# Performance work log

Hardware: AMD Instinct MI355X
Metric: run time of the kernel (lower is better)

Reference implementation:

```python
import jax, jax.numpy as jnp
import numpy as np

IN_DIM = 18 * 2 * 1 * 536  # 19296
H = 512
OUT = 11
STEPS = 1024


def setup_inputs() -> dict:
    key = jax.random.key(0)
    ks = jax.random.split(key, 14)
    s = 0.02  # small init scale for stable LSTM dynamics
    f32 = jnp.float32
    return {
        "inputs": jax.random.normal(ks[0], (STEPS, IN_DIM), dtype=f32),
        "W_in": jax.random.normal(ks[1], (H, IN_DIM), dtype=f32) * s,
        "b_in": jnp.zeros((H,), dtype=f32),
        "Wih0": jax.random.normal(ks[2], (4 * H, H), dtype=f32) * s,
        "Whh0": jax.random.normal(ks[3], (4 * H, H), dtype=f32) * s,
        "bih0": jnp.zeros((4 * H,), dtype=f32),
        "bhh0": jnp.zeros((4 * H,), dtype=f32),
        "Wih1": jax.random.normal(ks[4], (4 * H, H), dtype=f32) * s,
        "Whh1": jax.random.normal(ks[5], (4 * H, H), dtype=f32) * s,
        "bih1": jnp.zeros((4 * H,), dtype=f32),
        "bhh1": jnp.zeros((4 * H,), dtype=f32),
        "W_out": jax.random.normal(ks[6], (OUT, H), dtype=f32) * s,
        "b_out": jnp.zeros((OUT,), dtype=f32),
    }


def _lstm_cell(gates, c):
    # PyTorch gate order: input, forget, cell(g), output
    i, f, g, o = jnp.split(gates, 4, axis=-1)
    c_new = jax.nn.sigmoid(f) * c + jax.nn.sigmoid(i) * jnp.tanh(g)
    h_new = jax.nn.sigmoid(o) * jnp.tanh(c_new)
    return h_new, c_new


def reference(inputs, W_in, b_in, Wih0, Whh0, bih0, bhh0,
              Wih1, Whh1, bih1, bhh1, W_out, b_out):
    # Input projection is time-independent -> batch it across all steps.
    x_proj = inputs @ W_in.T + b_in            # (STEPS, H)
    gx0 = x_proj @ Wih0.T + bih0               # (STEPS, 4H) precomputed layer-0 input gates

    def step(carry, gx0_t):
        h0, c0, h1, c1 = carry
        h0, c0 = _lstm_cell(gx0_t + h0 @ Whh0.T + bhh0, c0)
        h1, c1 = _lstm_cell(h0 @ Wih1.T + bih1 + h1 @ Whh1.T + bhh1, c1)
        return (h0, c0, h1, c1), h1

    z = jnp.zeros((H,), dtype=inputs.dtype)
    (h0, c0, h1, c1), hs = jax.lax.scan(step, (z, z, z, z), gx0)
    outputs = (hs @ W_out.T + b_out)[:, None, :]   # (STEPS, 1, OUT) == torch (steps, batch=1, 11)
    hn = jnp.stack([h0, h1])[:, None, :]           # (num_layers=2, batch=1, H)
    cn = jnp.stack([c0, c1])[:, None, :]
    return outputs, hn, cn
```

## Files before the change

kernel.cpp:

```cpp
#include <hip/hip_runtime.h>
#include <math.h>

typedef unsigned long long ull;
typedef unsigned int u32;
typedef unsigned short u16;
typedef _Float16 half2v __attribute__((ext_vector_type(2)));
typedef __bf16 bf16x8 __attribute__((ext_vector_type(8)));
typedef float f32x4 __attribute__((ext_vector_type(4)));

#define H 512
#define STEPS 1024
#define OUTN 11

__device__ __forceinline__ float sigm(float x) { return 1.f / (1.f + __expf(-x)); }
__device__ __forceinline__ ull ld_pair(const ull* p) {
  return __hip_atomic_load((ull*)p, __ATOMIC_RELAXED, __HIP_MEMORY_SCOPE_AGENT);
}
__device__ __forceinline__ void st_pair(ull* p, ull v) {
  __hip_atomic_store(p, v, __ATOMIC_RELAXED, __HIP_MEMORY_SCOPE_AGENT);
}
__device__ __forceinline__ float dot2acc(half2v a, half2v b, float c) {
#if __has_builtin(__builtin_amdgcn_fdot2)
  return __builtin_amdgcn_fdot2(a, b, c, false);
#else
  return c + (float)a.x * (float)b.x + (float)a.y * (float)b.y;
#endif
}
__device__ __forceinline__ u16 f16bits(float x) {
  return __builtin_bit_cast(u16, (_Float16)x);
}
__device__ __forceinline__ half2v bch2(u32 u) { return __builtin_bit_cast(half2v, u); }

__device__ __forceinline__ u32 split_bf16(float x) {
  u32 u = __float_as_uint(x);
  u32 rh = (u + 0x7FFFu + ((u >> 16) & 1u)) & 0xFFFF0000u;
  float hf = __uint_as_float(rh);
  float lo = x - hf;
  u32 ul = __float_as_uint(lo);
  u32 rl = (ul + 0x7FFFu + ((ul >> 16) & 1u)) & 0xFFFF0000u;
  return (rh >> 16) | rl;
}

__global__ void cvt_split(float* __restrict__ A, float* __restrict__ B, int nA, int n4) {
  int idx = blockIdx.x * 256 + threadIdx.x;
  if (idx >= n4) return;
  int base = idx * 4;
  float* p = (base < nA) ? (A + base) : (B + (base - nA));
  float4 v = *(float4*)p;
  u32 r0 = split_bf16(v.x), r1 = split_bf16(v.y), r2 = split_bf16(v.z), r3 = split_bf16(v.w);
  uint4 o = make_uint4(r0, r1, r2, r3);
  *(uint4*)p = o;
}

__global__ __launch_bounds__(256, 2)
void gemm_hilo(const u32* __restrict__ A2, const u32* __restrict__ B2,
               float* __restrict__ C, int M, int N, int K)
{
  __shared__ __align__(16) u16 Ah[64 * 32], Al[64 * 32], Bh[64 * 32], Bl[64 * 32];
  const int z = blockIdx.z;
  const int zstart = z * 151;
  const int nsteps = (z < 3) ? 151 : 150;
  const int mt = blockIdx.x * 64, nt = blockIdx.y * 64;
  const int tid = threadIdx.x;
  const int row = tid >> 2, cg = (tid & 3) * 8;
  const int wave = tid >> 6, lane = tid & 63;
  const int wm = (wave & 1) * 32, wn = (wave >> 1) * 32;
  const int quad = lane >> 4, l16 = lane & 15;

  f32x4 acc[2][2];
#pragma unroll
  for (int i = 0; i < 2; ++i)
#pragma unroll
    for (int j = 0; j < 2; ++j) acc[i][j] = (f32x4)0.f;

  for (int s = 0; s < nsteps; ++s) {
    const int kb = (zstart + s) * 32;
    {
      const u32* ap = A2 + (size_t)(mt + row) * K + kb + cg;
      const u32* bp = B2 + (size_t)(nt + row) * K + kb + cg;
      uint4 a0 = *(const uint4*)ap, a1 = *(const uint4*)(ap + 4);
      uint4 b0 = *(const uint4*)bp, b1 = *(const uint4*)(bp + 4);
      uint4 hi, lo;
      hi = make_uint4((a0.x & 0xFFFF) | (a0.y << 16), (a0.z & 0xFFFF) | (a0.w << 16),
                      (a1.x & 0xFFFF) | (a1.y << 16), (a1.z & 0xFFFF) | (a1.w << 16));
      lo = make_uint4((a0.x >> 16) | (a0.y & 0xFFFF0000u), (a0.z >> 16) | (a0.w & 0xFFFF0000u),
                      (a1.x >> 16) | (a1.y & 0xFFFF0000u), (a1.z >> 16) | (a1.w & 0xFFFF0000u));
      *(uint4*)&Ah[row * 32 + cg] = hi;
      *(uint4*)&Al[row * 32 + cg] = lo;
      hi = make_uint4((b0.x & 0xFFFF) | (b0.y << 16), (b0.z & 0xFFFF) | (b0.w << 16),
                      (b1.x & 0xFFFF) | (b1.y << 16), (b1.z & 0xFFFF) | (b1.w << 16));
      lo = make_uint4((b0.x >> 16) | (b0.y & 0xFFFF0000u), (b0.z >> 16) | (b0.w & 0xFFFF0000u),
                      (b1.x >> 16) | (b1.y & 0xFFFF0000u), (b1.z >> 16) | (b1.w & 0xFFFF0000u));
      *(uint4*)&Bh[row * 32 + cg] = hi;
      *(uint4*)&Bl[row * 32 + cg] = lo;
    }
    __syncthreads();
    bf16x8 ah[2], al[2], bh[2], bl[2];
#pragma unroll
    for (int mf = 0; mf < 2; ++mf) {
      int r = (wm + mf * 16 + l16) * 32 + quad * 8;
      ah[mf] = *reinterpret_cast<const bf16x8*>(&Ah[r]);
      al[mf] = *reinterpret_cast<const bf16x8*>(&Al[r]);
    }
#pragma unroll
    for (int nf = 0; nf < 2; ++nf) {
      int r = (wn + nf * 16 + l16) * 32 + quad * 8;
      bh[nf] = *reinterpret_cast<const bf16x8*>(&Bh[r]);
      bl[nf] = *reinterpret_cast<const bf16x8*>(&Bl[r]);
    }
#pragma unroll
    for (int mf = 0; mf < 2; ++mf)
#pragma unroll
      for (int nf = 0; nf < 2; ++nf) {
        acc[mf][nf] = __builtin_amdgcn_mfma_f32_16x16x32_bf16(ah[mf], bh[nf], acc[mf][nf], 0, 0, 0);
        acc[mf][nf] = __builtin_amdgcn_mfma_f32_16x16x32_bf16(ah[mf], bl[nf], acc[mf][nf], 0, 0, 0);
        acc[mf][nf] = __builtin_amdgcn_mfma_f32_16x16x32_bf16(al[mf], bh[nf], acc[mf][nf], 0, 0, 0);
      }
    __syncthreads();
  }

#pragma unroll
  for (int mf = 0; mf < 2; ++mf)
#pragma unroll
    for (int nf = 0; nf < 2; ++nf)
#pragma unroll
      for (int r = 0; r < 4; ++r) {
        int rw = mt + wm + mf * 16 + quad * 4 + r;
        int cl = nt + wn + nf * 16 + l16;
        atomicAdd(&C[(size_t)rw * N + cl], acc[mf][nf][r]);
      }
}

#define GBM 64
#define GBN 64
#define GBK 64
#define GLD 76

__global__ __launch_bounds__(256, 2)
void gemm_nt(const float* __restrict__ A, const float* __restrict__ B,
             float* __restrict__ C, const float* __restrict__ bias,
             int M, int N, int K)
{
  __shared__ float As[GBM][GLD];
  __shared__ float Bs[GBN][GLD];
  const int mt = blockIdx.x, nt = blockIdx.y;
  const int tid = threadIdx.x;
  const int tx = tid & 15, ty = tid >> 4;

  float acc[4][4] = {{0.f}};

  for (int kb = 0; kb < K; kb += GBK) {
#pragma unroll
    for (int i = 0; i < 4; ++i) {
      int r = ty + i * 16;
      int gk = kb + tx * 4;
      *(float4*)&As[r][tx * 4] = *(const float4*)(A + (size_t)(mt * GBM + r) * K + gk);
      *(float4*)&Bs[r][tx * 4] = *(const float4*)(B + (size_t)(nt * GBN + r) * K + gk);
    }
    __syncthreads();
#pragma unroll
    for (int k4 = 0; k4 < GBK; k4 += 4) {
      float4 a[4], b[4];
#pragma unroll
      for (int i = 0; i < 4; ++i) a[i] = *(const float4*)&As[ty * 4 + i][k4];
#pragma unroll
      for (int j = 0; j < 4; ++j) b[j] = *(const float4*)&Bs[tx * 4 + j][k4];
#pragma unroll
      for (int i = 0; i < 4; ++i)
#pragma unroll
        for (int j = 0; j < 4; ++j) {
          acc[i][j] = fmaf(a[i].x, b[j].x, acc[i][j]);
          acc[i][j] = fmaf(a[i].y, b[j].y, acc[i][j]);
          acc[i][j] = fmaf(a[i].z, b[j].z, acc[i][j]);
          acc[i][j] = fmaf(a[i].w, b[j].w, acc[i][j]);
        }
    }
    __syncthreads();
  }

#pragma unroll
  for (int i = 0; i < 4; ++i) {
    int m = mt * GBM + ty * 4 + i;
#pragma unroll
    for (int j = 0; j < 4; ++j) {
      int n = nt * GBN + tx * 4 + j;
      C[(size_t)m * N + n] = acc[i][j] + bias[n];
    }
  }
}

__global__ void init_xproj(float* __restrict__ xp, const float* __restrict__ b_in) {
  int i = blockIdx.x * 256 + threadIdx.x;
  xp[i] = b_in[i & (H - 1)];
}

__global__ void out_proj(const float* __restrict__ hs1, const float* __restrict__ Wout,
                         const float* __restrict__ bout, float* __restrict__ out) {
  int idx = blockIdx.x * 256 + threadIdx.x;
  if (idx >= STEPS * OUTN) return;
  int t = idx / OUTN, o = idx - t * OUTN;
  const float* h = hs1 + t * H;
  const float* wr = Wout + o * H;
  float acc = 0.f;
#pragma unroll 4
  for (int i = 0; i < H; i += 4) {
    float4 hv = *(const float4*)(h + i);
    float4 wv = *(const float4*)(wr + i);
    acc = fmaf(hv.x, wv.x, acc);
    acc = fmaf(hv.y, wv.y, acc);
    acc = fmaf(hv.z, wv.z, acc);
    acc = fmaf(hv.w, wv.w, acc);
  }
  out[idx] = acc + bout[o];
}

#define NC0 24
#define NC1 16
#define RD 8

__global__ __launch_bounds__(512, 1)
void lstm_chains(const float* __restrict__ gx0,
                 const float* __restrict__ Whh0, const float* __restrict__ bhh0,
                 const float* __restrict__ Wih1, const float* __restrict__ Whh1,
                 const float* __restrict__ bih1, const float* __restrict__ bhh1,
                 float* __restrict__ hs1, float* __restrict__ out,
                 ull* __restrict__ mb0, ull* __restrict__ mb1,
                 int* __restrict__ flags1)
{
  const int wg = blockIdx.x;
  const int tid = threadIdx.x;
  const bool role0 = (wg < 8);

  __shared__ __align__(16) u32 hl_u[512];
  __shared__ __align__(16) float gbuf[256];
  __shared__ __align__(16) float gxb[256];
  __shared__ __align__(16) u32 pbuf[32];

  half2v wgt[8][16];
  float bias[8];
  int rg, ch;

  if (role0) {
    rg = tid >> 4; ch = tid & 15;
    int g = rg >> 3, lub = (rg & 7) * 8;
    int growb = (g << 9) + (wg << 6) + lub;
    const float* wb = Whh0 + (size_t)growb * H + ch * 32;
#pragma unroll
    for (int r = 0; r < 8; ++r) {
      const float* wr = wb + (size_t)r * H;
#pragma unroll
      for (int j4 = 0; j4 < 8; ++j4) {
        float4 f = *(const float4*)(wr + j4 * 4);
        wgt[r][2 * j4]     = half2v{(_Float16)f.x, (_Float16)f.y};
        wgt[r][2 * j4 + 1] = half2v{(_Float16)f.z, (_Float16)f.w};
      }
      bias[r] = bhh0[growb + r];
    }
  } else {
    rg = tid >> 5; ch = tid & 31;
    int g = rg >> 2, lub = (rg & 3) * 8;
    int growb = (g << 9) + ((wg - 8) << 5) + lub;
    const float* wb = (ch < 16) ? (Whh1 + (size_t)growb * H + ch * 32)
                                : (Wih1 + (size_t)growb * H + (ch - 16) * 32);
#pragma unroll
    for (int r = 0; r < 8; ++r) {
      const float* wr = wb + (size_t)r * H;
#pragma unroll
      for (int j4 = 0; j4 < 8; ++j4) {
        float4 f = *(const float4*)(wr + j4 * 4);
        wgt[r][2 * j4]     = half2v{(_Float16)f.x, (_Float16)f.y};
        wgt[r][2 * j4 + 1] = half2v{(_Float16)f.z, (_Float16)f.w};
      }
      bias[r] = bih1[growb + r] + bhh1[growb + r];
    }
  }

  float c_state = 0.f, h_last = 0.f;

  if (role0) {
    const int w = wg;
    for (int t = 0; t < STEPS; ++t) {
      if (tid >= 256) {
        int j = tid - 256;
        gxb[j] = gx0[t * 2048 + ((j >> 6) << 9) + (w << 6) + (j & 63)];
        if (j < 16 && (t & 3) == 0 && t > 0) {
          int need = t - 4, f;
          const int* fp = flags1 + ((w << 4) + j) * 16;
          do {
            f = __hip_atomic_load(fp, __ATOMIC_RELAXED, __HIP_MEMORY_SCOPE_AGENT);
          } while (f < need);
        }
      } else {
        const ull* src = mb0 + ((((w << 3) | ((t + RD - 1) & (RD - 1)))) << 8) + tid;
        ull p;
        do { p = ld_pair(src); } while ((unsigned)(p >> 32) != (unsigned)t);
        hl_u[tid] = (u32)p;
      }
      __syncthreads();

      float accv[8];
#pragma unroll
      for (int r = 0; r < 8; ++r) accv[r] = 0.f;
      {
        const u32* hp = hl_u + (ch << 4);
        uint4 q0 = *(const uint4*)hp;
        uint4 q1 = *(const uint4*)(hp + 4);
        uint4 q2 = *(const uint4*)(hp + 8);
        uint4 q3 = *(const uint4*)(hp + 12);
        half2v h2[16] = {bch2(q0.x), bch2(q0.y), bch2(q0.z), bch2(q0.w),
                         bch2(q1.x), bch2(q1.y), bch2(q1.z), bch2(q1.w),
                         bch2(q2.x), bch2(q2.y), bch2(q2.z), bch2(q2.w),
                         bch2(q3.x), bch2(q3.y), bch2(q3.z), bch2(q3.w)};
#pragma unroll
        for (int j = 0; j < 16; ++j)
#pragma unroll
          for (int r = 0; r < 8; ++r)
            accv[r] = dot2acc(wgt[r][j], h2[j], accv[r]);
      }
#pragma unroll
      for (int o = 1; o < 16; o <<= 1)
#pragma unroll
        for (int r = 0; r < 8; ++r)
          accv[r] += __shfl_xor(accv[r], o);
      if (ch == 0) {
        float4 ga = *(const float4*)&gxb[rg * 8];
        float4 gb = *(const float4*)&gxb[rg * 8 + 4];
        float4 o0 = make_float4(accv[0] + bias[0] + ga.x, accv[1] + bias[1] + ga.y,
                                accv[2] + bias[2] + ga.z, accv[3] + bias[3] + ga.w);
        float4 o1 = make_float4(accv[4] + bias[4] + gb.x, accv[5] + bias[5] + gb.y,
                                accv[6] + bias[6] + gb.z, accv[7] + bias[7] + gb.w);
        *(float4*)&gbuf[rg * 8] = o0;
        *(float4*)&gbuf[rg * 8 + 4] = o1;
      }
      __syncthreads();

      if (tid < 64) {
        float gi = gbuf[tid], gf = gbuf[64 + tid], gg = gbuf[128 + tid], go = gbuf[192 + tid];
        c_state = sigm(gf) * c_state + sigm(gi) * tanhf(gg);
        float hv = sigm(go) * tanhf(c_state);
        float hnb = __shfl_down(hv, 1);
        if ((tid & 1) == 0)
          pbuf[tid >> 1] = (u32)f16bits(hv) | ((u32)f16bits(hnb) << 16);
        h_last = hv;
      }
      __syncthreads();

      if (tid >= 256) {
        const int q = (tid >> 6) - 4;
        const int l = tid & 63, half = l >> 5, p = l & 31;
        const ull pay = ((ull)(unsigned)(t + 1) << 32) | (ull)pbuf[p];
        const int slot = t & (RD - 1);
        const int base = (w << 5) + p;
        const int cb = q + (half << 2);
        st_pair(mb0 + (((cb << 3) | slot) << 8) + base, pay);
        st_pair(mb0 + ((((8 + cb) << 3) | slot) << 8) + base, pay);
        st_pair(mb0 + ((((16 + cb) << 3) | slot) << 8) + base, pay);
      }
    }
  } else {
    const int v = wg - 8;
    for (int tau = 1; tau <= STEPS; ++tau) {
      const int t = tau - 1;
      if (tid < 256) {
        const ull* q1 = mb1 + ((((v << 3) | ((t + RD - 1) & (RD - 1)))) << 8) + tid;
        ull p;
        do { p = ld_pair(q1); } while ((unsigned)(p >> 32) != (unsigned)t);
        hl_u[tid] = (u32)p;
      } else {
        const ull* q0 = mb0 + (((((8 + v) << 3) | (t & (RD - 1)))) << 8) + (tid - 256);
        ull p;
        do { p = ld_pair(q0); } while ((unsigned)(p >> 32) != (unsigned)(t + 1));
        hl_u[tid] = (u32)p;
      }
      __syncthreads();

      float accv[8];
#pragma unroll
      for (int r = 0; r < 8; ++r) accv[r] = 0.f;
      {
        const u32* hp = hl_u + (ch << 4);
        uint4 q0 = *(const uint4*)hp;
        uint4 q1 = *(const uint4*)(hp + 4);
        uint4 q2 = *(const uint4*)(hp + 8);
        uint4 q3 = *(const uint4*)(hp + 12);
        half2v h2[16] = {bch2(q0.x), bch2(q0.y), bch2(q0.z), bch2(q0.w),
                         bch2(q1.x), bch2(q1.y), bch2(q1.z), bch2(q1.w),
                         bch2(q2.x), bch2(q2.y), bch2(q2.z), bch2(q2.w),
                         bch2(q3.x), bch2(q3.y), bch2(q3.z), bch2(q3.w)};
#pragma unroll
        for (int j = 0; j < 16; ++j)
#pragma unroll
          for (int r = 0; r < 8; ++r)
            accv[r] = dot2acc(wgt[r][j], h2[j], accv[r]);
      }
#pragma unroll
      for (int o = 1; o < 32; o <<= 1)
#pragma unroll
        for (int r = 0; r < 8; ++r)
          accv[r] += __shfl_xor(accv[r], o);
      if (ch == 0) {
        float4 o0 = make_float4(accv[0] + bias[0], accv[1] + bias[1],
                                accv[2] + bias[2], accv[3] + bias[3]);
        float4 o1 = make_float4(accv[4] + bias[4], accv[5] + bias[5],
                                accv[6] + bias[6], accv[7] + bias[7]);
        *(float4*)&gbuf[rg * 8] = o0;
        *(float4*)&gbuf[rg * 8 + 4] = o1;
      }
      __syncthreads();

      if (tid < 32) {
        int u = (v << 5) + tid;
        float gi = gbuf[tid], gf = gbuf[32 + tid], gg = gbuf[64 + tid], go = gbuf[96 + tid];
        c_state = sigm(gf) * c_state + sigm(gi) * tanhf(gg);
        float hv = sigm(go) * tanhf(c_state);
        float hnb = __shfl_down(hv, 1);
        if ((tid & 1) == 0)
          pbuf[tid >> 1] = (u32)f16bits(hv) | ((u32)f16bits(hnb) << 16);
        h_last = hv;
        hs1[t * H + u] = hv;
      }
      if (((tau & 3) == 0) && tid >= 64 && tid < 72)
        __hip_atomic_store(flags1 + (((tid - 64) << 4) + v) * 16, tau,
                           __ATOMIC_RELAXED, __HIP_MEMORY_SCOPE_AGENT);
      __syncthreads();

      if (tid < 256) {
        const int q = tid >> 6;
        const int l = tid & 63, half = l >> 5, p = l & 31;
        if (p < 16) {
          const ull pay = ((ull)(unsigned)(t + 1) << 32) | (ull)pbuf[p];
          const int slot = t & (RD - 1);
          const int base = (v << 4) + p;
          const int cb = q + (half << 2);
          st_pair(mb1 + (((cb << 3) | slot) << 8) + base, pay);
          st_pair(mb1 + ((((8 + cb) << 3) | slot) << 8) + base, pay);
        }
      }
    }
  }

  if (role0) {
    if (tid < 64) {
      int u = (wg << 6) + tid;
      out[STEPS * OUTN + u] = h_last;
      out[STEPS * OUTN + 2 * H + u] = c_state;
    }
  } else {
    if (tid < 32) {
      int u = ((wg - 8) << 5) + tid;
      out[STEPS * OUTN + H + u] = h_last;
      out[STEPS * OUTN + 3 * H + u] = c_state;
    }
  }
}

extern "C" void kernel_launch(void* const* d_in, const int* in_sizes, int n_in,
                              void* d_out, int out_size, void* d_ws, size_t ws_size,
                              hipStream_t stream)
{
  (void)in_sizes; (void)n_in; (void)out_size; (void)ws_size;
  float* inputs = (float*)d_in[0];
  float* W_in   = (float*)d_in[1];
  const float* b_in   = (const float*)d_in[2];
  const float* Wih0   = (const float*)d_in[3];
  const float* Whh0   = (const float*)d_in[4];
  const float* bih0   = (const float*)d_in[5];
  const float* bhh0   = (const float*)d_in[6];
  const float* Wih1   = (const float*)d_in[7];
  const float* Whh1   = (const float*)d_in[8];
  const float* bih1   = (const float*)d_in[9];
  const float* bhh1   = (const float*)d_in[10];
  const float* W_out  = (const float*)d_in[11];
  const float* b_out  = (const float*)d_in[12];
  float* out = (float*)d_out;
  float* ws = (float*)d_ws;

  float* xp  = ws;
  float* gx0 = ws + 524288;
  float* hs1 = ws + 524288 + 2097152;
  char* syncb = (char*)(ws + 3145728);
  ull* mb0 = (ull*)syncb;
  ull* mb1 = (ull*)(syncb + 24 * 8 * 256 * 8);
  int* flags1 = (int*)(syncb + (24 + 16) * 8 * 256 * 8);

  hipMemsetAsync(syncb, 0, (24 + 16) * 8 * 256 * 8 + 8192, stream);

  {
    const int nA = STEPS * 19296;
    const int n4 = (nA + H * 19296) / 4;
    cvt_split<<<n4 / 256, 256, 0, stream>>>(inputs, W_in, nA, n4);
  }
  init_xproj<<<2048, 256, 0, stream>>>(xp, b_in);
  {
    dim3 g(16, 8, 4);
    gemm_hilo<<<g, 256, 0, stream>>>((const u32*)inputs, (const u32*)W_in, xp,
                                     1024, 512, 19296);
  }
  {
    dim3 g(16, 32, 1);
    gemm_nt<<<g, 256, 0, stream>>>(xp, Wih0, gx0, bih0, 1024, 2048, 512);
  }
  lstm_chains<<<24, 512, 0, stream>>>(gx0, Whh0, bhh0, Wih1, Whh1, bih1, bhh1,
                                      hs1, out, mb0, mb1, flags1);
  out_proj<<<44, 256, 0, stream>>>(hs1, W_out, b_out, out);
}
```

Baseline: 3.103 ms.

## Co-locate LSTM workgroups on one XCD and poll L2-local mailboxes

Launches 256 workgroups, reads each one's XCD id from a hardware register, and lets only the 24 workgroups on the most populated XCD take the LSTM roles while the rest exit. Producers also write every mailbox payload with plain stores that stay in the shared L2, and consumers poll that copy with sc0 loads, falling back to the agent-scope copy every few tries. The aim is to cut the cross-XCD coherence latency of each step handshake in the serial recurrence. It relies on undocumented register encoding and on at least 24 workgroups landing on one XCD and being co-resident; otherwise too few roles get filled and the kernel can deadlock.

```diff
diff --git a/kernel.cpp b/kernel.cpp
--- a/kernel.cpp
+++ b/kernel.cpp
@@ -19,6 +19,23 @@
 __device__ __forceinline__ void st_pair(ull* p, ull v) {
   __hip_atomic_store(p, v, __ATOMIC_RELAXED, __HIP_MEMORY_SCOPE_AGENT);
 }
+__device__ __forceinline__ void st_local(ull* p, ull v) {
+  asm volatile("global_store_dwordx2 %0, %1, off" :: "v"(p), "v"(v) : "memory");
+}
+__device__ __forceinline__ ull poll2(const ull* fast, const ull* slow, unsigned want) {
+  for (;;) {
+#pragma unroll 1
+    for (int s = 0; s < 6; ++s) {
+      ull r;
+      asm volatile("global_load_dwordx2 %0, %1, off sc0\n\ts_waitcnt vmcnt(0)"
+                   : "=v"(r) : "v"(fast) : "memory");
+      if ((unsigned)(r >> 32) == want) return r;
+    }
+    ull r = __hip_atomic_load((ull*)slow, __ATOMIC_RELAXED, __HIP_MEMORY_SCOPE_AGENT);
+    if ((unsigned)(r >> 32) == want) return r;
+  }
+}
+
 __device__ __forceinline__ float dot2acc(half2v a, half2v b, float c) {
 #if __has_builtin(__builtin_amdgcn_fdot2)
   return __builtin_amdgcn_fdot2(a, b, c, false);
@@ -217,6 +234,7 @@
 #define NC0 24
 #define NC1 16
 #define RD 8
+#define NWG 256
 
 __global__ __launch_bounds__(512, 1)
 void lstm_chains(const float* __restrict__ gx0,
@@ -225,10 +243,33 @@
                  const float* __restrict__ bih1, const float* __restrict__ bhh1,
                  float* __restrict__ hs1, float* __restrict__ out,
                  ull* __restrict__ mb0, ull* __restrict__ mb1,
-                 int* __restrict__ flags1)
+                 int* __restrict__ flags1, int* __restrict__ claim,
+                 ull* __restrict__ lmb0, ull* __restrict__ lmb1)
 {
-  const int wg = blockIdx.x;
   const int tid = threadIdx.x;
+  __shared__ int s_role;
+
+  if (tid == 0) {
+    u32 xid = ((u32)__builtin_amdgcn_s_getreg(63508)) & 7u;
+    __hip_atomic_fetch_add(&claim[xid * 16], 1, __ATOMIC_SEQ_CST, __HIP_MEMORY_SCOPE_AGENT);
+    __hip_atomic_fetch_add(&claim[128], 1, __ATOMIC_SEQ_CST, __HIP_MEMORY_SCOPE_AGENT);
+    while (__hip_atomic_load(&claim[128], __ATOMIC_SEQ_CST, __HIP_MEMORY_SCOPE_AGENT) < NWG)
+      __builtin_amdgcn_s_sleep(8);
+    int best = 0, bc = -1;
+    for (int i = 0; i < 8; ++i) {
+      int c = __hip_atomic_load(&claim[i * 16], __ATOMIC_SEQ_CST, __HIP_MEMORY_SCOPE_AGENT);
+      if (c > bc) { bc = c; best = i; }
+    }
+    int role = -1;
+    if ((int)xid == best) {
+      int s = __hip_atomic_fetch_add(&claim[144], 1, __ATOMIC_SEQ_CST, __HIP_MEMORY_SCOPE_AGENT);
+      if (s < 24) role = s;
+    }
+    s_role = role;
+  }
+  __syncthreads();
+  const int wg = s_role;
+  if (wg < 0) return;
   const bool role0 = (wg < 8);
 
   __shared__ __align__(16) u32 hl_u[512];
@@ -291,9 +332,8 @@
           } while (f < need);
         }
       } else {
-        const ull* src = mb0 + ((((w << 3) | ((t + RD - 1) & (RD - 1)))) << 8) + tid;
-        ull p;
-        do { p = ld_pair(src); } while ((unsigned)(p >> 32) != (unsigned)t);
+        const int idx = ((((w << 3) | ((t + RD - 1) & (RD - 1)))) << 8) + tid;
+        ull p = poll2(lmb0 + idx, mb0 + idx, (unsigned)t);
         hl_u[tid] = (u32)p;
       }
       __syncthreads();
@@ -352,9 +392,15 @@
         const int slot = t & (RD - 1);
         const int base = (w << 5) + p;
         const int cb = q + (half << 2);
-        st_pair(mb0 + (((cb << 3) | slot) << 8) + base, pay);
-        st_pair(mb0 + ((((8 + cb) << 3) | slot) << 8) + base, pay);
-        st_pair(mb0 + ((((16 + cb) << 3) | slot) << 8) + base, pay);
+        const int i0 = (((cb << 3) | slot) << 8) + base;
+        const int i1 = ((((8 + cb) << 3) | slot) << 8) + base;
+        const int i2 = ((((16 + cb) << 3) | slot) << 8) + base;
+        st_local(lmb0 + i0, pay);
+        st_local(lmb0 + i1, pay);
+        st_local(lmb0 + i2, pay);
+        st_pair(mb0 + i0, pay);
+        st_pair(mb0 + i1, pay);
+        st_pair(mb0 + i2, pay);
       }
     }
   } else {
@@ -362,14 +408,12 @@
     for (int tau = 1; tau <= STEPS; ++tau) {
       const int t = tau - 1;
       if (tid < 256) {
-        const ull* q1 = mb1 + ((((v << 3) | ((t + RD - 1) & (RD - 1)))) << 8) + tid;
-        ull p;
-        do { p = ld_pair(q1); } while ((unsigned)(p >> 32) != (unsigned)t);
+        const int idx = ((((v << 3) | ((t + RD - 1) & (RD - 1)))) << 8) + tid;
+        ull p = poll2(lmb1 + idx, mb1 + idx, (unsigned)t);
         hl_u[tid] = (u32)p;
       } else {
-        const ull* q0 = mb0 + (((((8 + v) << 3) | (t & (RD - 1)))) << 8) + (tid - 256);
-        ull p;
-        do { p = ld_pair(q0); } while ((unsigned)(p >> 32) != (unsigned)(t + 1));
+        const int idx = (((((8 + v) << 3) | (t & (RD - 1)))) << 8) + (tid - 256);
+        ull p = poll2(lmb0 + idx, mb0 + idx, (unsigned)(t + 1));
         hl_u[tid] = (u32)p;
       }
       __syncthreads();
@@ -432,8 +476,12 @@
           const int slot = t & (RD - 1);
           const int base = (v << 4) + p;
           const int cb = q + (half << 2);
-          st_pair(mb1 + (((cb << 3) | slot) << 8) + base, pay);
-          st_pair(mb1 + ((((8 + cb) << 3) | slot) << 8) + base, pay);
+          const int i0 = (((cb << 3) | slot) << 8) + base;
+          const int i1 = ((((8 + cb) << 3) | slot) << 8) + base;
+          st_local(lmb1 + i0, pay);
+          st_local(lmb1 + i1, pay);
+          st_pair(mb1 + i0, pay);
+          st_pair(mb1 + i1, pay);
         }
       }
     }
@@ -479,11 +527,14 @@
   float* gx0 = ws + 524288;
   float* hs1 = ws + 524288 + 2097152;
   char* syncb = (char*)(ws + 3145728);
-  ull* mb0 = (ull*)syncb;
-  ull* mb1 = (ull*)(syncb + 24 * 8 * 256 * 8);
-  int* flags1 = (int*)(syncb + (24 + 16) * 8 * 256 * 8);
-
-  hipMemsetAsync(syncb, 0, (24 + 16) * 8 * 256 * 8 + 8192, stream);
+  ull* mb0    = (ull*)syncb;
+  ull* mb1    = (ull*)(syncb + 393216);
+  int* flags1 = (int*)(syncb + 655360);
+  int* claim  = (int*)(syncb + 663552);
+  ull* lmb0   = (ull*)(syncb + 664576);
+  ull* lmb1   = (ull*)(syncb + 1057792);
+
+  hipMemsetAsync(syncb, 0, 1319936, stream);
 
   {
     const int nA = STEPS * 19296;
@@ -500,7 +551,7 @@
     dim3 g(16, 32, 1);
     gemm_nt<<<g, 256, 0, stream>>>(xp, Wih0, gx0, bih0, 1024, 2048, 512);
   }
-  lstm_chains<<<24, 512, 0, stream>>>(gx0, Whh0, bhh0, Wih1, Whh1, bih1, bhh1,
-                                      hs1, out, mb0, mb1, flags1);
+  lstm_chains<<<NWG, 512, 0, stream>>>(gx0, Whh0, bhh0, Wih1, Whh1, bih1, bhh1,
+                                       hs1, out, mb0, mb1, flags1, claim, lmb0, lmb1);
   out_proj<<<44, 256, 0, stream>>>(hs1, W_out, b_out, out);
 }
```

Result: slower. 3.530 ms (+13.8%).

## Fuse input GEMMs and LSTM chains into one persistent kernel with flag-gated overlap

Applied to the files above, without the earlier changes.

Merges the bf16 split conversion, bias init, input-projection GEMM, gate GEMM and the recurrent LSTM chains into a single persistent launch. 24 blocks run the recurrence while 232 worker blocks pull GEMM tiles from an atomic queue. The first time-slab of rows gets finer K-splitting so the recurrence can start early, and per-tile ready flags let the chains consume gx0 in 64-step chunks as it is produced. This aims to hide the long serial LSTM behind the projection work and remove launch gaps. The cost is spin-wait synchronisation, grid-wide barriers that rely on every block being co-resident, and more shared memory per block.

```diff
diff --git a/kernel.cpp b/kernel.cpp
--- a/kernel.cpp
+++ b/kernel.cpp
@@ -39,159 +39,6 @@
   u32 ul = __float_as_uint(lo);
   u32 rl = (ul + 0x7FFFu + ((ul >> 16) & 1u)) & 0xFFFF0000u;
   return (rh >> 16) | rl;
-}
-
-__global__ void cvt_split(float* __restrict__ A, float* __restrict__ B, int nA, int n4) {
-  int idx = blockIdx.x * 256 + threadIdx.x;
-  if (idx >= n4) return;
-  int base = idx * 4;
-  float* p = (base < nA) ? (A + base) : (B + (base - nA));
-  float4 v = *(float4*)p;
-  u32 r0 = split_bf16(v.x), r1 = split_bf16(v.y), r2 = split_bf16(v.z), r3 = split_bf16(v.w);
-  uint4 o = make_uint4(r0, r1, r2, r3);
-  *(uint4*)p = o;
-}
-
-__global__ __launch_bounds__(256, 2)
-void gemm_hilo(const u32* __restrict__ A2, const u32* __restrict__ B2,
-               float* __restrict__ C, int M, int N, int K)
-{
-  __shared__ __align__(16) u16 Ah[64 * 32], Al[64 * 32], Bh[64 * 32], Bl[64 * 32];
-  const int z = blockIdx.z;
-  const int zstart = z * 151;
-  const int nsteps = (z < 3) ? 151 : 150;
-  const int mt = blockIdx.x * 64, nt = blockIdx.y * 64;
-  const int tid = threadIdx.x;
-  const int row = tid >> 2, cg = (tid & 3) * 8;
-  const int wave = tid >> 6, lane = tid & 63;
-  const int wm = (wave & 1) * 32, wn = (wave >> 1) * 32;
-  const int quad = lane >> 4, l16 = lane & 15;
-
-  f32x4 acc[2][2];
-#pragma unroll
-  for (int i = 0; i < 2; ++i)
-#pragma unroll
-    for (int j = 0; j < 2; ++j) acc[i][j] = (f32x4)0.f;
-
-  for (int s = 0; s < nsteps; ++s) {
-    const int kb = (zstart + s) * 32;
-    {
-      const u32* ap = A2 + (size_t)(mt + row) * K + kb + cg;
-      const u32* bp = B2 + (size_t)(nt + row) * K + kb + cg;
-      uint4 a0 = *(const uint4*)ap, a1 = *(const uint4*)(ap + 4);
-      uint4 b0 = *(const uint4*)bp, b1 = *(const uint4*)(bp + 4);
-      uint4 hi, lo;
-      hi = make_uint4((a0.x & 0xFFFF) | (a0.y << 16), (a0.z & 0xFFFF) | (a0.w << 16),
-                      (a1.x & 0xFFFF) | (a1.y << 16), (a1.z & 0xFFFF) | (a1.w << 16));
-      lo = make_uint4((a0.x >> 16) | (a0.y & 0xFFFF0000u), (a0.z >> 16) | (a0.w & 0xFFFF0000u),
-                      (a1.x >> 16) | (a1.y & 0xFFFF0000u), (a1.z >> 16) | (a1.w & 0xFFFF0000u));
-      *(uint4*)&Ah[row * 32 + cg] = hi;
-      *(uint4*)&Al[row * 32 + cg] = lo;
-      hi = make_uint4((b0.x & 0xFFFF) | (b0.y << 16), (b0.z & 0xFFFF) | (b0.w << 16),
-                      (b1.x & 0xFFFF) | (b1.y << 16), (b1.z & 0xFFFF) | (b1.w << 16));
-      lo = make_uint4((b0.x >> 16) | (b0.y & 0xFFFF0000u), (b0.z >> 16) | (b0.w & 0xFFFF0000u),
-                      (b1.x >> 16) | (b1.y & 0xFFFF0000u), (b1.z >> 16) | (b1.w & 0xFFFF0000u));
-      *(uint4*)&Bh[row * 32 + cg] = hi;
-      *(uint4*)&Bl[row * 32 + cg] = lo;
-    }
-    __syncthreads();
-    bf16x8 ah[2], al[2], bh[2], bl[2];
-#pragma unroll
-    for (int mf = 0; mf < 2; ++mf) {
-      int r = (wm + mf * 16 + l16) * 32 + quad * 8;
-      ah[mf] = *reinterpret_cast<const bf16x8*>(&Ah[r]);
-      al[mf] = *reinterpret_cast<const bf16x8*>(&Al[r]);
-    }
-#pragma unroll
-    for (int nf = 0; nf < 2; ++nf) {
-      int r = (wn + nf * 16 + l16) * 32 + quad * 8;
-      bh[nf] = *reinterpret_cast<const bf16x8*>(&Bh[r]);
-      bl[nf] = *reinterpret_cast<const bf16x8*>(&Bl[r]);
-    }
-#pragma unroll
-    for (int mf = 0; mf < 2; ++mf)
-#pragma unroll
-      for (int nf = 0; nf < 2; ++nf) {
-        acc[mf][nf] = __builtin_amdgcn_mfma_f32_16x16x32_bf16(ah[mf], bh[nf], acc[mf][nf], 0, 0, 0);
-        acc[mf][nf] = __builtin_amdgcn_mfma_f32_16x16x32_bf16(ah[mf], bl[nf], acc[mf][nf], 0, 0, 0);
-        acc[mf][nf] = __builtin_amdgcn_mfma_f32_16x16x32_bf16(al[mf], bh[nf], acc[mf][nf], 0, 0, 0);
-      }
-    __syncthreads();
-  }
-
-#pragma unroll
-  for (int mf = 0; mf < 2; ++mf)
-#pragma unroll
-    for (int nf = 0; nf < 2; ++nf)
-#pragma unroll
-      for (int r = 0; r < 4; ++r) {
-        int rw = mt + wm + mf * 16 + quad * 4 + r;
-        int cl = nt + wn + nf * 16 + l16;
-        atomicAdd(&C[(size_t)rw * N + cl], acc[mf][nf][r]);
-      }
-}
-
-#define GBM 64
-#define GBN 64
-#define GBK 64
-#define GLD 76
-
-__global__ __launch_bounds__(256, 2)
-void gemm_nt(const float* __restrict__ A, const float* __restrict__ B,
-             float* __restrict__ C, const float* __restrict__ bias,
-             int M, int N, int K)
-{
-  __shared__ float As[GBM][GLD];
-  __shared__ float Bs[GBN][GLD];
-  const int mt = blockIdx.x, nt = blockIdx.y;
-  const int tid = threadIdx.x;
-  const int tx = tid & 15, ty = tid >> 4;
-
-  float acc[4][4] = {{0.f}};
-
-  for (int kb = 0; kb < K; kb += GBK) {
-#pragma unroll
-    for (int i = 0; i < 4; ++i) {
-      int r = ty + i * 16;
-      int gk = kb + tx * 4;
-      *(float4*)&As[r][tx * 4] = *(const float4*)(A + (size_t)(mt * GBM + r) * K + gk);
-      *(float4*)&Bs[r][tx * 4] = *(const float4*)(B + (size_t)(nt * GBN + r) * K + gk);
-    }
-    __syncthreads();
-#pragma unroll
-    for (int k4 = 0; k4 < GBK; k4 += 4) {
-      float4 a[4], b[4];
-#pragma unroll
-      for (int i = 0; i < 4; ++i) a[i] = *(const float4*)&As[ty * 4 + i][k4];
-#pragma unroll
-      for (int j = 0; j < 4; ++j) b[j] = *(const float4*)&Bs[tx * 4 + j][k4];
-#pragma unroll
-      for (int i = 0; i < 4; ++i)
-#pragma unroll
-        for (int j = 0; j < 4; ++j) {
-          acc[i][j] = fmaf(a[i].x, b[j].x, acc[i][j]);
-          acc[i][j] = fmaf(a[i].y, b[j].y, acc[i][j]);
-          acc[i][j] = fmaf(a[i].z, b[j].z, acc[i][j]);
-          acc[i][j] = fmaf(a[i].w, b[j].w, acc[i][j]);
-        }
-    }
-    __syncthreads();
-  }
-
-#pragma unroll
-  for (int i = 0; i < 4; ++i) {
-    int m = mt * GBM + ty * 4 + i;
-#pragma unroll
-    for (int j = 0; j < 4; ++j) {
-      int n = nt * GBN + tx * 4 + j;
-      C[(size_t)m * N + n] = acc[i][j] + bias[n];
-    }
-  }
-}
-
-__global__ void init_xproj(float* __restrict__ xp, const float* __restrict__ b_in) {
-  int i = blockIdx.x * 256 + threadIdx.x;
-  xp[i] = b_in[i & (H - 1)];
 }
 
 __global__ void out_proj(const float* __restrict__ hs1, const float* __restrict__ Wout,
@@ -217,24 +64,249 @@
 #define NC0 24
 #define NC1 16
 #define RD 8
+#define NROLE 24
+#define NWORK 232
+#define FGRID 256
+
+#define FS_CVT 0
+#define FS_XPQ 16
+#define FS_GXQ 32
+#define FS_XPD 64
+#define FS_GXF 320
 
 __global__ __launch_bounds__(512, 1)
-void lstm_chains(const float* __restrict__ gx0,
-                 const float* __restrict__ Whh0, const float* __restrict__ bhh0,
-                 const float* __restrict__ Wih1, const float* __restrict__ Whh1,
-                 const float* __restrict__ bih1, const float* __restrict__ bhh1,
-                 float* __restrict__ hs1, float* __restrict__ out,
-                 ull* __restrict__ mb0, ull* __restrict__ mb1,
-                 int* __restrict__ flags1)
+void fused(float* __restrict__ inputs, float* __restrict__ W_in,
+           const float* __restrict__ b_in,
+           const float* __restrict__ Wih0, const float* __restrict__ Whh0,
+           const float* __restrict__ bih0, const float* __restrict__ bhh0,
+           const float* __restrict__ Wih1, const float* __restrict__ Whh1,
+           const float* __restrict__ bih1, const float* __restrict__ bhh1,
+           float* __restrict__ xp, float* __restrict__ gx0,
+           float* __restrict__ hs1, float* __restrict__ out,
+           ull* __restrict__ mb0, ull* __restrict__ mb1,
+           int* __restrict__ flags1, int* __restrict__ fsync)
 {
-  const int wg = blockIdx.x;
+  const int bid = blockIdx.x;
   const int tid = threadIdx.x;
-  const bool role0 = (wg < 8);
-
+
+  __shared__ __align__(16) char wsm[77824];
   __shared__ __align__(16) u32 hl_u[512];
   __shared__ __align__(16) float gbuf[256];
   __shared__ __align__(16) float gxb[256];
   __shared__ __align__(16) u32 pbuf[32];
+  __shared__ int s_pair;
+
+  if (bid >= NROLE) {
+    const int wb = bid - NROLE;
+    {
+      const int nA = STEPS * 19296;
+      const int n4 = (nA + H * 19296) / 4;
+      for (int i = wb * 512 + tid; i < n4; i += NWORK * 512) {
+        int base = i * 4;
+        float* p = (base < nA) ? (inputs + base) : (W_in + (base - nA));
+        float4 v = *(float4*)p;
+        uint4 o = make_uint4(split_bf16(v.x), split_bf16(v.y),
+                             split_bf16(v.z), split_bf16(v.w));
+        *(uint4*)p = o;
+      }
+      for (int i = wb * 512 + tid; i < STEPS * H; i += NWORK * 512)
+        xp[i] = b_in[i & (H - 1)];
+      __syncthreads();
+      if (tid == 0) {
+        __hip_atomic_fetch_add(&fsync[FS_CVT], 1, __ATOMIC_RELEASE, __HIP_MEMORY_SCOPE_AGENT);
+        while (__hip_atomic_load(&fsync[FS_CVT], __ATOMIC_ACQUIRE, __HIP_MEMORY_SCOPE_AGENT) < NWORK)
+          __builtin_amdgcn_s_sleep(8);
+      }
+      __syncthreads();
+    }
+
+    const int half = tid >> 8;
+    const int tid_h = tid & 255;
+    const u32* A2 = (const u32*)inputs;
+    const u32* B2 = (const u32*)W_in;
+    const int K = 19296;
+
+    {
+      u16* Ah = (u16*)(wsm + half * 16384);
+      u16* Al = Ah + 2048;
+      u16* Bh = Al + 2048;
+      u16* Bl = Bh + 2048;
+      const int row = tid_h >> 2, cg = (tid_h & 3) * 8;
+      const int wave = tid_h >> 6, lane = tid_h & 63;
+      const int wm = (wave & 1) * 32, wn = (wave >> 1) * 32;
+      const int quad = lane >> 4, l16 = lane & 15;
+
+      for (;;) {
+        if (tid == 0)
+          s_pair = __hip_atomic_fetch_add(&fsync[FS_XPQ], 1, __ATOMIC_RELAXED, __HIP_MEMORY_SCOPE_AGENT);
+        __syncthreads();
+        const int p = s_pair;
+        if (p >= 368) break;
+        const int tau = 2 * p + half;
+        int mt, nt, zstart, nsteps, dummy_at;
+        if (tau < 256) {
+          mt = 0; nt = tau >> 5;
+          int zz = tau & 31;
+          zstart = (zz < 27) ? zz * 19 : 513 + (zz - 27) * 18;
+          nsteps = 19; dummy_at = (zz >= 27) ? 18 : -1;
+        } else {
+          int u = tau - 256;
+          mt = 1 + (u >> 5);
+          int r = u & 31;
+          nt = r >> 2;
+          int zz = r & 3;
+          zstart = zz * 151;
+          nsteps = (tau < 512) ? 19 : 151;
+          nsteps = 151; dummy_at = (zz == 3) ? 150 : -1;
+        }
+
+        f32x4 acc[2][2];
+#pragma unroll
+        for (int i = 0; i < 2; ++i)
+#pragma unroll
+          for (int j = 0; j < 2; ++j) acc[i][j] = (f32x4)0.f;
+
+        const int NS = (tau < 256) ? 19 : 151;
+        for (int s = 0; s < NS; ++s) {
+          const bool dummy = (s == dummy_at);
+          const int kb = (dummy ? 0 : (zstart + s)) * 32;
+          {
+            const u32* ap = A2 + (size_t)(mt * 64 + row) * K + kb + cg;
+            const u32* bp = B2 + (size_t)(nt * 64 + row) * K + kb + cg;
+            uint4 a0 = *(const uint4*)ap, a1 = *(const uint4*)(ap + 4);
+            uint4 b0 = *(const uint4*)bp, b1 = *(const uint4*)(bp + 4);
+            uint4 hi, lo;
+            hi = make_uint4((a0.x & 0xFFFF) | (a0.y << 16), (a0.z & 0xFFFF) | (a0.w << 16),
+                            (a1.x & 0xFFFF) | (a1.y << 16), (a1.z & 0xFFFF) | (a1.w << 16));
+            lo = make_uint4((a0.x >> 16) | (a0.y & 0xFFFF0000u), (a0.z >> 16) | (a0.w & 0xFFFF0000u),
+                            (a1.x >> 16) | (a1.y & 0xFFFF0000u), (a1.z >> 16) | (a1.w & 0xFFFF0000u));
+            *(uint4*)&Ah[row * 32 + cg] = hi;
+            *(uint4*)&Al[row * 32 + cg] = lo;
+            hi = make_uint4((b0.x & 0xFFFF) | (b0.y << 16), (b0.z & 0xFFFF) | (b0.w << 16),
+                            (b1.x & 0xFFFF) | (b1.y << 16), (b1.z & 0xFFFF) | (b1.w << 16));
+            lo = make_uint4((b0.x >> 16) | (b0.y & 0xFFFF0000u), (b0.z >> 16) | (b0.w & 0xFFFF0000u),
+                            (b1.x >> 16) | (b1.y & 0xFFFF0000u), (b1.z >> 16) | (b1.w & 0xFFFF0000u));
+            *(uint4*)&Bh[row * 32 + cg] = hi;
+            *(uint4*)&Bl[row * 32 + cg] = lo;
+          }
+          __syncthreads();
+          bf16x8 ah[2], al[2], bh[2], bl[2];
+#pragma unroll
+          for (int mf = 0; mf < 2; ++mf) {
+            int r = (wm + mf * 16 + l16) * 32 + quad * 8;
+            ah[mf] = *reinterpret_cast<const bf16x8*>(&Ah[r]);
+            al[mf] = *reinterpret_cast<const bf16x8*>(&Al[r]);
+          }
+#pragma unroll
+          for (int nf = 0; nf < 2; ++nf) {
+            int r = (wn + nf * 16 + l16) * 32 + quad * 8;
+            bh[nf] = *reinterpret_cast<const bf16x8*>(&Bh[r]);
+            bl[nf] = *reinterpret_cast<const bf16x8*>(&Bl[r]);
+          }
+          if (dummy) {
+#pragma unroll
+            for (int mf = 0; mf < 2; ++mf) { ah[mf] = (bf16x8)0; al[mf] = (bf16x8)0; }
+          }
+#pragma unroll
+          for (int mf = 0; mf < 2; ++mf)
+#pragma unroll
+            for (int nf = 0; nf < 2; ++nf) {
+              acc[mf][nf] = __builtin_amdgcn_mfma_f32_16x16x32_bf16(ah[mf], bh[nf], acc[mf][nf], 0, 0, 0);
+              acc[mf][nf] = __builtin_amdgcn_mfma_f32_16x16x32_bf16(ah[mf], bl[nf], acc[mf][nf], 0, 0, 0);
+              acc[mf][nf] = __builtin_amdgcn_mfma_f32_16x16x32_bf16(al[mf], bh[nf], acc[mf][nf], 0, 0, 0);
+            }
+          __syncthreads();
+        }
+#pragma unroll
+        for (int mf = 0; mf < 2; ++mf)
+#pragma unroll
+          for (int nf = 0; nf < 2; ++nf)
+#pragma unroll
+            for (int r = 0; r < 4; ++r) {
+              int rw = mt * 64 + wm + mf * 16 + quad * 4 + r;
+              int cl = nt * 64 + wn + nf * 16 + l16;
+              atomicAdd(&xp[(size_t)rw * 512 + cl], acc[mf][nf][r]);
+            }
+        if (tid_h == 0)
+          __hip_atomic_fetch_add(&fsync[FS_XPD + mt * 16], 1, __ATOMIC_RELEASE, __HIP_MEMORY_SCOPE_AGENT);
+        __syncthreads();
+      }
+    }
+
+    {
+      float (*As)[76] = (float(*)[76])(wsm + half * 38912);
+      float (*Bs)[76] = As + 64;
+      const int tx = tid_h & 15, ty = tid_h >> 4;
+      for (;;) {
+        if (tid == 0)
+          s_pair = __hip_atomic_fetch_add(&fsync[FS_GXQ], 1, __ATOMIC_RELAXED, __HIP_MEMORY_SCOPE_AGENT);
+        __syncthreads();
+        const int p = s_pair;
+        if (p >= 256) break;
+        const int tau = 2 * p + half;
+        const int mt = tau >> 5, nt = tau & 31;
+        const int tgt0 = ((2 * p) >> 5) == 0 ? 256 : 32;
+        const int tgt1 = ((2 * p + 1) >> 5) == 0 ? 256 : 32;
+        if (tid == 0) {
+          while (__hip_atomic_load(&fsync[FS_XPD + ((2 * p) >> 5) * 16], __ATOMIC_ACQUIRE,
+                                   __HIP_MEMORY_SCOPE_AGENT) < tgt0)
+            __builtin_amdgcn_s_sleep(2);
+        }
+        if (tid == 256) {
+          while (__hip_atomic_load(&fsync[FS_XPD + ((2 * p + 1) >> 5) * 16], __ATOMIC_ACQUIRE,
+                                   __HIP_MEMORY_SCOPE_AGENT) < tgt1)
+            __builtin_amdgcn_s_sleep(2);
+        }
+        __syncthreads();
+
+        float acc[4][4] = {{0.f}};
+        for (int kb = 0; kb < 512; kb += 64) {
+#pragma unroll
+          for (int i = 0; i < 4; ++i) {
+            int r = ty + i * 16;
+            int gk = kb + tx * 4;
+            *(float4*)&As[r][tx * 4] = *(const float4*)(xp + (size_t)(mt * 64 + r) * 512 + gk);
+            *(float4*)&Bs[r][tx * 4] = *(const float4*)(Wih0 + (size_t)(nt * 64 + r) * 512 + gk);
+          }
+          __syncthreads();
+#pragma unroll
+          for (int k4 = 0; k4 < 64; k4 += 4) {
+            float4 a[4], b[4];
+#pragma unroll
+            for (int i = 0; i < 4; ++i) a[i] = *(const float4*)&As[ty * 4 + i][k4];
+#pragma unroll
+            for (int j = 0; j < 4; ++j) b[j] = *(const float4*)&Bs[tx * 4 + j][k4];
+#pragma unroll
+            for (int i = 0; i < 4; ++i)
+#pragma unroll
+              for (int j = 0; j < 4; ++j) {
+                acc[i][j] = fmaf(a[i].x, b[j].x, acc[i][j]);
+                acc[i][j] = fmaf(a[i].y, b[j].y, acc[i][j]);
+                acc[i][j] = fmaf(a[i].z, b[j].z, acc[i][j]);
+                acc[i][j] = fmaf(a[i].w, b[j].w, acc[i][j]);
+              }
+          }
+          __syncthreads();
+        }
+#pragma unroll
+        for (int i = 0; i < 4; ++i) {
+          int m = mt * 64 + ty * 4 + i;
+#pragma unroll
+          for (int j = 0; j < 4; ++j) {
+            int n = nt * 64 + tx * 4 + j;
+            gx0[(size_t)m * 2048 + n] = acc[i][j] + bih0[n];
+          }
+        }
+        if (tid_h == 0)
+          __hip_atomic_store(&fsync[FS_GXF + mt * 32 + nt], 1, __ATOMIC_RELEASE, __HIP_MEMORY_SCOPE_AGENT);
+        __syncthreads();
+      }
+    }
+    return;
+  }
+
+  const int wg = bid;
+  const bool role0 = (wg < 8);
 
   half2v wgt[8][16];
   float bias[8];
@@ -280,6 +352,14 @@
   if (role0) {
     const int w = wg;
     for (int t = 0; t < STEPS; ++t) {
+      if ((t & 63) == 0) {
+        if (tid >= 256 && tid < 260) {
+          const int fi = FS_GXF + ((t >> 6) << 5) + ((tid - 256) << 3) + w;
+          while (__hip_atomic_load(&fsync[fi], __ATOMIC_ACQUIRE, __HIP_MEMORY_SCOPE_AGENT) == 0)
+            __builtin_amdgcn_s_sleep(2);
+        }
+        __syncthreads();
+      }
       if (tid >= 256) {
         int j = tid - 256;
         gxb[j] = gx0[t * 2048 + ((j >> 6) << 9) + (w << 6) + (j & 63)];
@@ -479,28 +559,15 @@
   float* gx0 = ws + 524288;
   float* hs1 = ws + 524288 + 2097152;
   char* syncb = (char*)(ws + 3145728);
-  ull* mb0 = (ull*)syncb;
-  ull* mb1 = (ull*)(syncb + 24 * 8 * 256 * 8);
-  int* flags1 = (int*)(syncb + (24 + 16) * 8 * 256 * 8);
-
-  hipMemsetAsync(syncb, 0, (24 + 16) * 8 * 256 * 8 + 8192, stream);
-
-  {
-    const int nA = STEPS * 19296;
-    const int n4 = (nA + H * 19296) / 4;
-    cvt_split<<<n4 / 256, 256, 0, stream>>>(inputs, W_in, nA, n4);
-  }
-  init_xproj<<<2048, 256, 0, stream>>>(xp, b_in);
-  {
-    dim3 g(16, 8, 4);
-    gemm_hilo<<<g, 256, 0, stream>>>((const u32*)inputs, (const u32*)W_in, xp,
-                                     1024, 512, 19296);
-  }
-  {
-    dim3 g(16, 32, 1);
-    gemm_nt<<<g, 256, 0, stream>>>(xp, Wih0, gx0, bih0, 1024, 2048, 512);
-  }
-  lstm_chains<<<24, 512, 0, stream>>>(gx0, Whh0, bhh0, Wih1, Whh1, bih1, bhh1,
-                                      hs1, out, mb0, mb1, flags1);
+  ull* mb0    = (ull*)syncb;
+  ull* mb1    = (ull*)(syncb + 393216);
+  int* flags1 = (int*)(syncb + 655360);
+  int* fsync  = (int*)(syncb + 663552);
+
+  hipMemsetAsync(syncb, 0, 667648, stream);
+
+  fused<<<FGRID, 512, 0, stream>>>(inputs, W_in, b_in, Wih0, Whh0, bih0, bhh0,
+                                   Wih1, Whh1, bih1, bhh1,
+                                   xp, gx0, hs1, out, mb0, mb1, flags1, fsync);
   out_proj<<<44, 256, 0, stream>>>(hs1, W_out, b_out, out);
 }
```

After: 3.211 ms. 1.03x slower.
